# Kernel tuning notes

Hardware: AMD Instinct MI355X
Metric: run time of the kernel (lower is better)

The kernel has to match this reference:

```python
import jax, jax.numpy as jnp
import numpy as np

V, B, T, C, H, L = 32000, 4, 1024, 1024, 16, 8
HS = C // H  # head_size = 64


def _ln(x, g, b):
    m = x.mean(-1, keepdims=True)
    v = x.var(-1, keepdims=True)
    return (x - m) / jnp.sqrt(v + 1e-5) * g + b


def setup_inputs() -> dict:
    key = jax.random.key(0)
    ks = jax.random.split(key, 24)
    s = 0.02
    inp = {
        "idx": jax.random.randint(ks[0], (B, T), 0, V, dtype=jnp.int64),
        "tok_emb": jax.random.normal(ks[1], (V, C), jnp.float32) * s,
        "pos_emb": jax.random.normal(ks[2], (T, C), jnp.float32) * s,
        "Wq": jax.random.normal(ks[3], (L, H, C, HS), jnp.float32) * s,
        "Wk": jax.random.normal(ks[4], (L, H, C, HS), jnp.float32) * s,
        "Wv": jax.random.normal(ks[5], (L, H, C, HS), jnp.float32) * s,
        "Ph_w": jax.random.normal(ks[6], (L, H, HS, C), jnp.float32) * s,
        "Ph_b": jnp.zeros((L, H, C), jnp.float32),
        "Pm_w": jax.random.normal(ks[7], (L, C, C), jnp.float32) * s,
        "Pm_b": jnp.zeros((L, C), jnp.float32),
        "ln1_g": jnp.ones((L, C), jnp.float32),
        "ln1_b": jnp.zeros((L, C), jnp.float32),
        "ln2_g": jnp.ones((L, C), jnp.float32),
        "ln2_b": jnp.zeros((L, C), jnp.float32),
        "W1": jax.random.normal(ks[8], (L, C, 4 * C), jnp.float32) * s,
        "b1": jnp.zeros((L, 4 * C), jnp.float32),
        "W2": jax.random.normal(ks[9], (L, 4 * C, C), jnp.float32) * s,
        "b2": jnp.zeros((L, C), jnp.float32),
        "lnf_g": jnp.ones((C,), jnp.float32),
        "lnf_b": jnp.zeros((C,), jnp.float32),
        "head_w": jax.random.normal(ks[10], (C, V), jnp.float32) * s,
        "head_b": jnp.zeros((V,), jnp.float32),
    }
    return inp


def reference(idx, tok_emb, pos_emb, Wq, Wk, Wv, Ph_w, Ph_b, Pm_w, Pm_b,
              ln1_g, ln1_b, ln2_g, ln2_b, W1, b1, W2, b2, lnf_g, lnf_b,
              head_w, head_b):
    Bx, Tx = idx.shape
    x = tok_emb[idx] + pos_emb[:Tx]  # [B,T,C]
    mask = jnp.tril(jnp.ones((Tx, Tx), bool))
    scale = x.shape[-1] ** -0.5  # NOTE: original scales by n_embd**-0.5, not head_size
    n_layers = Wq.shape[0]
    for l in range(n_layers):
        xn = _ln(x, ln1_g[l], ln1_b[l])
        q = jnp.einsum('btc,hcs->bhts', xn, Wq[l])
        k = jnp.einsum('btc,hcs->bhts', xn, Wk[l])
        v = jnp.einsum('btc,hcs->bhts', xn, Wv[l])
        wei = jnp.einsum('bhts,bhus->bhtu', q, k) * scale
        wei = jnp.where(mask, wei, -jnp.inf)
        wei = jax.nn.softmax(wei, axis=-1)
        o = jnp.einsum('bhtu,bhus->bhts', wei, v)  # [B,H,T,HS]
        per = jnp.einsum('bhts,hsc->bhtc', o, Ph_w[l]) + Ph_b[l][None, :, None, :]
        sa = per.sum(axis=1) @ Pm_w[l] + Pm_b[l]  # combine heads, final proj
        x = x + sa
        xn2 = _ln(x, ln2_g[l], ln2_b[l])
        h = jax.nn.gelu(xn2 @ W1[l] + b1[l], approximate=False)
        x = x + h @ W2[l] + b2[l]
    x = _ln(x, lnf_g, lnf_b)
    return x @ head_w + head_b  # logits [B,T,V]
```

## Files before the change

kernel.cpp:

```cpp
#include <hip/hip_runtime.h>
#include <hip/hip_bf16.h>
#include <math.h>

static constexpr int V = 32000, B = 4, T = 1024, C = 1024, H = 16, NL = 8, HS = 64;
static constexpr int M = B * T;

typedef __bf16 bf16x8 __attribute__((ext_vector_type(8)));
typedef __bf16 bf16x4 __attribute__((ext_vector_type(4)));
typedef float f32x4 __attribute__((ext_vector_type(4)));

#define AS1 __attribute__((address_space(1)))
#define AS3 __attribute__((address_space(3)))

__global__ void k_embed(const int* __restrict__ idx, const float* __restrict__ tok,
                        const float* __restrict__ pos, float* __restrict__ x) {
  int g = blockIdx.x * blockDim.x + threadIdx.x;
  if (g >= M * C / 4) return;
  int c4 = g & 255;
  int bt = g >> 8;
  int t = bt & (T - 1);
  int row = idx[bt];
  float4 tv = *(const float4*)(tok + (size_t)row * C + c4 * 4);
  float4 pv = *(const float4*)(pos + (size_t)t * C + c4 * 4);
  float4 o;
  o.x = tv.x + pv.x; o.y = tv.y + pv.y; o.z = tv.z + pv.z; o.w = tv.w + pv.w;
  *(float4*)(x + (size_t)bt * C + c4 * 4) = o;
}

__global__ __launch_bounds__(256) void k_ln_bf(const float* __restrict__ x, const float* __restrict__ g,
                                               const float* __restrict__ b, __hip_bfloat16* __restrict__ y) {
  int row = blockIdx.x, tid = threadIdx.x;
  float4 v = ((const float4*)(x + (size_t)row * C))[tid];
  float s = v.x + v.y + v.z + v.w;
  float ss = v.x * v.x + v.y * v.y + v.z * v.z + v.w * v.w;
  for (int off = 32; off > 0; off >>= 1) {
    s += __shfl_down(s, off);
    ss += __shfl_down(ss, off);
  }
  __shared__ float sb[4], qb[4];
  int wid = tid >> 6;
  if ((tid & 63) == 0) { sb[wid] = s; qb[wid] = ss; }
  __syncthreads();
  float st = sb[0] + sb[1] + sb[2] + sb[3];
  float qt = qb[0] + qb[1] + qb[2] + qb[3];
  float mean = st * (1.0f / C);
  float var = qt * (1.0f / C) - mean * mean;
  float rstd = rsqrtf(var + 1e-5f);
  float4 gv = ((const float4*)g)[tid];
  float4 bv = ((const float4*)b)[tid];
  union { __hip_bfloat16 h[4]; ushort4 u; } pk;
  pk.h[0] = __float2bfloat16((v.x - mean) * rstd * gv.x + bv.x);
  pk.h[1] = __float2bfloat16((v.y - mean) * rstd * gv.y + bv.y);
  pk.h[2] = __float2bfloat16((v.z - mean) * rstd * gv.z + bv.z);
  pk.h[3] = __float2bfloat16((v.w - mean) * rstd * gv.w + bv.w);
  *(ushort4*)(y + (size_t)row * C + tid * 4) = pk.u;
}

__device__ __forceinline__ void transp_block(const float* __restrict__ in, __hip_bfloat16* __restrict__ out,
                                             int K, int N, int bx, int by, float (*t)[65]) {
  int n0 = bx * 64, k0 = by * 64;
  int tx = threadIdx.x & 15, ty = threadIdx.x >> 4;
#pragma unroll
  for (int i = 0; i < 64; i += 16) {
    float4 v = *(const float4*)(in + (size_t)(k0 + ty + i) * N + n0 + tx * 4);
    t[ty + i][tx * 4 + 0] = v.x;
    t[ty + i][tx * 4 + 1] = v.y;
    t[ty + i][tx * 4 + 2] = v.z;
    t[ty + i][tx * 4 + 3] = v.w;
  }
  __syncthreads();
#pragma unroll
  for (int i = 0; i < 64; i += 16) {
    int n = ty + i;
    union { __hip_bfloat16 h[4]; ushort4 u; } pk;
#pragma unroll
    for (int j = 0; j < 4; ++j) pk.h[j] = __float2bfloat16(t[tx * 4 + j][n]);
    *(ushort4*)(out + (size_t)(n0 + n) * K + k0 + tx * 4) = pk.u;
  }
}

__global__ __launch_bounds__(256) void k_transp(const float* __restrict__ in, __hip_bfloat16* __restrict__ out,
                                                int K, int N) {
  __shared__ float t[64][65];
  transp_block(in, out, K, N, blockIdx.x, blockIdx.y, t);
}

__global__ __launch_bounds__(256) void k_prep(const float* __restrict__ Wq, const float* __restrict__ Wk,
                                              const float* __restrict__ Wv, const float* __restrict__ Pm,
                                              const float* __restrict__ Ph, const float* __restrict__ W1,
                                              const float* __restrict__ W2,
                                              __hip_bfloat16* __restrict__ qkvw, __hip_bfloat16* __restrict__ pmT,
                                              __hip_bfloat16* __restrict__ phB, __hip_bfloat16* __restrict__ w1T,
                                              __hip_bfloat16* __restrict__ w2T) {
  __shared__ float tls[64][65];
  int bid = blockIdx.x;
  if (bid < 768) {
    int bx = bid & 15, z = bid >> 4;
    int sel = z >> 4, h = z & 15;
    const float* W = sel == 0 ? Wq : (sel == 1 ? Wk : Wv);
    const float* in = W + (size_t)h * C * HS;
    __hip_bfloat16* o = qkvw + ((size_t)sel * 1024 + h * 64) * C;
    int k0 = bx * 64;
    int tx = threadIdx.x & 15, ty = threadIdx.x >> 4;
#pragma unroll
    for (int i = 0; i < 64; i += 16) {
      float4 v = *(const float4*)(in + (size_t)(k0 + ty + i) * HS + tx * 4);
      tls[ty + i][tx * 4 + 0] = v.x;
      tls[ty + i][tx * 4 + 1] = v.y;
      tls[ty + i][tx * 4 + 2] = v.z;
      tls[ty + i][tx * 4 + 3] = v.w;
    }
    __syncthreads();
#pragma unroll
    for (int i = 0; i < 64; i += 16) {
      int n = ty + i;
      union { __hip_bfloat16 h4[4]; ushort4 u; } pk;
#pragma unroll
      for (int j = 0; j < 4; ++j) pk.h4[j] = __float2bfloat16(tls[tx * 4 + j][n]);
      *(ushort4*)(o + (size_t)n * C + k0 + tx * 4) = pk.u;
    }
  } else if (bid < 1024) {
    int r = bid - 768;
    transp_block(Pm, pmT, C, C, r & 15, r >> 4, tls);
  } else if (bid < 2048) {
    int g = (bid - 1024) * 256 + threadIdx.x;
    float4 v = ((const float4*)Ph)[g];
    union { __hip_bfloat16 h[4]; ushort4 u; } pk;
    pk.h[0] = __float2bfloat16(v.x);
    pk.h[1] = __float2bfloat16(v.y);
    pk.h[2] = __float2bfloat16(v.z);
    pk.h[3] = __float2bfloat16(v.w);
    ((ushort4*)phB)[g] = pk.u;
  } else if (bid < 3072) {
    int r = bid - 2048;
    transp_block(W1, w1T, C, 4 * C, r & 63, r >> 6, tls);
  } else {
    int r = bid - 3072;
    transp_block(W2, w2T, 4 * C, C, r & 15, r >> 4, tls);
  }
}

__global__ __launch_bounds__(256) void k_biasc(const float* __restrict__ phb, const float* __restrict__ Pm,
                                               const float* __restrict__ Pmb, float* __restrict__ bc) {
  __shared__ float bs[1024];
  __shared__ float red[4][64];
  int tid = threadIdx.x;
#pragma unroll
  for (int q = 0; q < 4; ++q) {
    int c = tid * 4 + q;
    float s = 0.0f;
    for (int h = 0; h < H; ++h) s += phb[(size_t)h * C + c];
    bs[c] = s;
  }
  __syncthreads();
  int c = blockIdx.x * 64 + (tid & 63);
  int part = tid >> 6;
  float s = 0.0f;
  for (int j = part * 256; j < part * 256 + 256; ++j) s += bs[j] * Pm[(size_t)j * C + c];
  red[part][tid & 63] = s;
  __syncthreads();
  if (tid < 64)
    bc[blockIdx.x * 64 + tid] = Pmb[blockIdx.x * 64 + tid] + red[0][tid] + red[1][tid] + red[2][tid] + red[3][tid];
}

template <int BIAS, int GELU, int RES, int OUTBF>
__global__ __launch_bounds__(256) void k_gemm_bf(const __hip_bfloat16* __restrict__ A,
                                                 const __hip_bfloat16* __restrict__ Bt,
                                                 void* Cout, const float* __restrict__ bias,
                                                 const float* res, int N, int K) {
  __shared__ __align__(16) __hip_bfloat16 As[128 * 32];
  __shared__ __align__(16) __hip_bfloat16 Bs[128 * 32];
  int bm = blockIdx.y * 128, bn = blockIdx.x * 128;
  int tid = threadIdx.x;
  int w = tid >> 6, l = tid & 63;
  int wr = (w >> 1) * 64, wc = (w & 1) * 64;
  int lr = l >> 2;
  int lk = (l & 3) * 8;
  int fr = l & 15;
  int fk = (l >> 4) * 8;
  const __hip_bfloat16* Ag = A + (size_t)bm * K;
  const __hip_bfloat16* Bg = Bt + (size_t)bn * K;
  f32x4 acc[4][4];
#pragma unroll
  for (int m = 0; m < 4; ++m)
#pragma unroll
    for (int n = 0; n < 4; ++n) acc[m][n] = (f32x4){0.f, 0.f, 0.f, 0.f};

  for (int k0 = 0; k0 < K; k0 += 32) {
    __syncthreads();
#pragma unroll
    for (int i = 0; i < 2; ++i) {
      int seg = w * 2 + i;
      int r = seg * 16 + lr;
      __builtin_amdgcn_global_load_lds((const AS1 void*)(Ag + (size_t)r * K + k0 + lk),
                                       (AS3 void*)(As + seg * 512), 16, 0, 0);
      __builtin_amdgcn_global_load_lds((const AS1 void*)(Bg + (size_t)r * K + k0 + lk),
                                       (AS3 void*)(Bs + seg * 512), 16, 0, 0);
    }
    __syncthreads();
    bf16x8 af[4], bfr[4];
#pragma unroll
    for (int m = 0; m < 4; ++m) af[m] = *(const bf16x8*)(As + ((size_t)(wr + m * 16 + fr)) * 32 + fk);
#pragma unroll
    for (int n = 0; n < 4; ++n) bfr[n] = *(const bf16x8*)(Bs + ((size_t)(wc + n * 16 + fr)) * 32 + fk);
#pragma unroll
    for (int m = 0; m < 4; ++m)
#pragma unroll
      for (int n = 0; n < 4; ++n)
        acc[m][n] = __builtin_amdgcn_mfma_f32_16x16x32_bf16(af[m], bfr[n], acc[m][n], 0, 0, 0);
  }
  int crow0 = (l >> 4) * 4;
  int ccol = l & 15;
#pragma unroll
  for (int m = 0; m < 4; ++m) {
    int row = bm + wr + m * 16 + crow0;
#pragma unroll
    for (int n = 0; n < 4; ++n) {
      int col = bn + wc + n * 16 + ccol;
      float bv = BIAS ? bias[col] : 0.0f;
#pragma unroll
      for (int r = 0; r < 4; ++r) {
        float v = acc[m][n][r] + bv;
        if (GELU) v = 0.5f * v * (1.0f + erff(v * 0.70710678118f));
        if (RES) v += res[(size_t)(row + r) * N + col];
        if (OUTBF)
          ((__hip_bfloat16*)Cout)[(size_t)(row + r) * N + col] = __float2bfloat16(v);
        else
          ((float*)Cout)[(size_t)(row + r) * N + col] = v;
      }
    }
  }
}

template <int BIAS, int GELU, int RES, int OUTBF>
__global__ __launch_bounds__(512, 2) void k_gemm256(const __hip_bfloat16* __restrict__ Ah,
                                                    const __hip_bfloat16* __restrict__ Bth,
                                                    void* Cout, const float* __restrict__ bias,
                                                    const float* res, int N, int K) {
  __shared__ __align__(16) __bf16 As[3][256 * 32];
  __shared__ __align__(16) __bf16 Bs[3][256 * 32];
  const __bf16* A = (const __bf16*)Ah;
  const __bf16* Bt = (const __bf16*)Bth;
  const int nx = N >> 8;
  const int bid = blockIdx.x;
  const int sw = ((bid & 7) * ((int)gridDim.x >> 3)) + (bid >> 3);
  const int bn = (sw % nx) << 8;
  const int bm = (sw / nx) << 8;
  const int tid = threadIdx.x, w = tid >> 6, l = tid & 63;
  const int wm = w >> 2, wn = w & 3;
  const int fr = l & 15, fg = l >> 4;
  const int srow = w * 32 + (l >> 2);
  const int scole = ((((l & 3) << 4) ^ ((l & 8) << 2) ^ (l & 16)) >> 1);
  const __bf16* Ag = A + (size_t)(bm + srow) * K + scole;
  const __bf16* Bg = Bt + (size_t)(bn + srow) * K + scole;
  const int arow = wm * 128 + fr;
  const int brow = wn * 64 + fr;
  const int koff = (((fg * 16) ^ (((fr & 2) << 4) | ((fr & 4) << 2))) >> 1);

  f32x4 acc[8][4];
#pragma unroll
  for (int m = 0; m < 8; ++m)
#pragma unroll
    for (int n = 0; n < 4; ++n) acc[m][n] = (f32x4){0.f, 0.f, 0.f, 0.f};

  auto stage = [&](int bufi, int tt) {
    size_t kb = (size_t)tt * 32;
#pragma unroll
    for (int jj = 0; jj < 2; ++jj) {
      __builtin_amdgcn_global_load_lds((const AS1 void*)(Ag + (size_t)jj * 16 * K + kb),
                                       (AS3 void*)(&As[bufi][(w * 32 + jj * 16) * 32]), 16, 0, 0);
      __builtin_amdgcn_global_load_lds((const AS1 void*)(Bg + (size_t)jj * 16 * K + kb),
                                       (AS3 void*)(&Bs[bufi][(w * 32 + jj * 16) * 32]), 16, 0, 0);
    }
  };

  const int NT = K >> 5;
  stage(0, 0);
  stage(1, 1);
  asm volatile("s_waitcnt vmcnt(4)" ::: "memory");
  __builtin_amdgcn_sched_barrier(0);
  __builtin_amdgcn_s_barrier();
  __builtin_amdgcn_sched_barrier(0);

  int cb = 0;
  for (int t = 0; t < NT; ++t) {
    int pb = cb + 2 >= 3 ? cb - 1 : cb + 2;
    if (t + 2 < NT) stage(pb, t + 2);
    bf16x8 fa[8], fb[4];
#pragma unroll
    for (int mg = 0; mg < 8; ++mg) fa[mg] = *(const bf16x8*)(&As[cb][(arow + mg * 16) * 32 + koff]);
#pragma unroll
    for (int ng = 0; ng < 4; ++ng) fb[ng] = *(const bf16x8*)(&Bs[cb][(brow + ng * 16) * 32 + koff]);
    __builtin_amdgcn_s_setprio(1);
#pragma unroll
    for (int mg = 0; mg < 8; ++mg)
#pragma unroll
      for (int ng = 0; ng < 4; ++ng)
        acc[mg][ng] = __builtin_amdgcn_mfma_f32_16x16x32_bf16(fa[mg], fb[ng], acc[mg][ng], 0, 0, 0);
    __builtin_amdgcn_s_setprio(0);
    if (t + 2 < NT)
      asm volatile("s_waitcnt vmcnt(4)" ::: "memory");
    else
      asm volatile("s_waitcnt vmcnt(0)" ::: "memory");
    __builtin_amdgcn_sched_barrier(0);
    __builtin_amdgcn_s_barrier();
    __builtin_amdgcn_sched_barrier(0);
    cb = cb + 1 >= 3 ? 0 : cb + 1;
  }

#pragma unroll
  for (int mg = 0; mg < 8; ++mg) {
    int row = bm + wm * 128 + mg * 16 + fg * 4;
#pragma unroll
    for (int n = 0; n < 4; ++n) {
      int col = bn + wn * 64 + n * 16 + fr;
      float bvx = BIAS ? bias[col] : 0.0f;
#pragma unroll
      for (int r = 0; r < 4; ++r) {
        float v = acc[mg][n][r] + bvx;
        if (GELU) v = 0.5f * v * (1.0f + erff(v * 0.70710678118f));
        if (RES) v += res[(size_t)(row + r) * N + col];
        if (OUTBF)
          ((__hip_bfloat16*)Cout)[(size_t)(row + r) * N + col] = __float2bfloat16(v);
        else
          ((float*)Cout)[(size_t)(row + r) * N + col] = v;
      }
    }
  }
}

__global__ __launch_bounds__(256) void k_attn(const __hip_bfloat16* __restrict__ qkvh,
                                              __hip_bfloat16* __restrict__ o) {
  const __bf16* qkv = (const __bf16*)qkvh;
  int qi = blockIdx.x;
  int bh = blockIdx.y;
  int b = bh >> 4, h = bh & 15;
  int tid = threadIdx.x;
  int w = tid >> 6, l = tid & 63;
  int fr = l & 15, fg = l >> 4;
  int qw = qi * 64 + w * 16;

  __shared__ __align__(16) __bf16 Ks[32][72];
  __shared__ __align__(16) __bf16 Vs[32][76];
  __shared__ __align__(16) __bf16 Ps[4][16][40];

  const size_t bT = (size_t)b * T;
  bf16x8 a_q[2];
  {
    const __bf16* qp = qkv + (bT + qw + fr) * 3072 + h * 64 + fg * 8;
    a_q[0] = *(const bf16x8*)qp;
    a_q[1] = *(const bf16x8*)(qp + 32);
  }
  f32x4 acc_o[4];
#pragma unroll
  for (int n = 0; n < 4; ++n) acc_o[n] = (f32x4){0.f, 0.f, 0.f, 0.f};
  float mrow[4] = {-1e30f, -1e30f, -1e30f, -1e30f};
  float lrow[4] = {0.f, 0.f, 0.f, 0.f};

  int sr = tid >> 3;
  int sc = (tid & 7) * 8;
  int ntile = (qi + 1) * 2;
  for (int t = 0; t < ntile; ++t) {
    int kv0 = t * 32;
    __syncthreads();
    {
      const __bf16* kp = qkv + (bT + kv0 + sr) * 3072 + 1024 + h * 64 + sc;
      bf16x8 k8 = *(const bf16x8*)kp;
      bf16x8 v8 = *(const bf16x8*)(kp + 1024);
      *(bf16x8*)&Ks[sr][sc] = k8;
      *(bf16x4*)&Vs[sr][sc] = __builtin_shufflevector(v8, v8, 0, 1, 2, 3);
      *(bf16x4*)&Vs[sr][sc + 4] = __builtin_shufflevector(v8, v8, 4, 5, 6, 7);
    }
    __syncthreads();
    if (kv0 > qw + 15) continue;

    f32x4 s0 = (f32x4){0.f, 0.f, 0.f, 0.f}, s1 = s0;
    s0 = __builtin_amdgcn_mfma_f32_16x16x32_bf16(a_q[0], *(const bf16x8*)&Ks[fr][fg * 8], s0, 0, 0, 0);
    s0 = __builtin_amdgcn_mfma_f32_16x16x32_bf16(a_q[1], *(const bf16x8*)&Ks[fr][32 + fg * 8], s0, 0, 0, 0);
    s1 = __builtin_amdgcn_mfma_f32_16x16x32_bf16(a_q[0], *(const bf16x8*)&Ks[16 + fr][fg * 8], s1, 0, 0, 0);
    s1 = __builtin_amdgcn_mfma_f32_16x16x32_bf16(a_q[1], *(const bf16x8*)&Ks[16 + fr][32 + fg * 8], s1, 0, 0, 0);

    int qrow = qw + fg * 4;
#pragma unroll
    for (int r = 0; r < 4; ++r) { s0[r] *= 0.03125f; s1[r] *= 0.03125f; }
    if (kv0 + 31 > qw) {
#pragma unroll
      for (int r = 0; r < 4; ++r) {
        if (kv0 + fr > qrow + r) s0[r] = -1e30f;
        if (kv0 + 16 + fr > qrow + r) s1[r] = -1e30f;
      }
    }
    float tm[4], psum[4], alpha[4];
#pragma unroll
    for (int r = 0; r < 4; ++r) tm[r] = fmaxf(s0[r], s1[r]);
#pragma unroll
    for (int off = 1; off < 16; off <<= 1)
#pragma unroll
      for (int r = 0; r < 4; ++r) tm[r] = fmaxf(tm[r], __shfl_xor(tm[r], off));
#pragma unroll
    for (int r = 0; r < 4; ++r) {
      float mnew = fmaxf(mrow[r], tm[r]);
      alpha[r] = __expf(mrow[r] - mnew);
      mrow[r] = mnew;
      float p0 = __expf(s0[r] - mnew);
      float p1 = __expf(s1[r] - mnew);
      s0[r] = p0; s1[r] = p1;
      psum[r] = p0 + p1;
    }
#pragma unroll
    for (int off = 1; off < 16; off <<= 1)
#pragma unroll
      for (int r = 0; r < 4; ++r) psum[r] += __shfl_xor(psum[r], off);
#pragma unroll
    for (int r = 0; r < 4; ++r) lrow[r] = lrow[r] * alpha[r] + psum[r];
#pragma unroll
    for (int n = 0; n < 4; ++n)
#pragma unroll
      for (int r = 0; r < 4; ++r) acc_o[n][r] *= alpha[r];

#pragma unroll
    for (int r = 0; r < 4; ++r) {
      Ps[w][fg * 4 + r][fr] = (__bf16)s0[r];
      Ps[w][fg * 4 + r][16 + fr] = (__bf16)s1[r];
    }
    bf16x8 a_p = *(const bf16x8*)&Ps[w][fr][fg * 8];
#pragma unroll
    for (int n = 0; n < 4; ++n) {
      bf16x8 bvv;
#pragma unroll
      for (int j = 0; j < 8; ++j) bvv[j] = Vs[fg * 8 + j][n * 16 + fr];
      acc_o[n] = __builtin_amdgcn_mfma_f32_16x16x32_bf16(a_p, bvv, acc_o[n], 0, 0, 0);
    }
  }
  float inv[4];
#pragma unroll
  for (int r = 0; r < 4; ++r) inv[r] = 1.0f / lrow[r];
  __bf16* ob = (__bf16*)o;
#pragma unroll
  for (int n = 0; n < 4; ++n)
#pragma unroll
    for (int r = 0; r < 4; ++r)
      ob[(bT + qw + fg * 4 + r) * 1024 + h * 64 + n * 16 + fr] = (__bf16)(acc_o[n][r] * inv[r]);
}

extern "C" void kernel_launch(void* const* d_in, const int* in_sizes, int n_in,
                              void* d_out, int out_size, void* d_ws, size_t ws_size,
                              hipStream_t stream) {
  const int* idx = (const int*)d_in[0];
  const float* tok = (const float*)d_in[1];
  const float* pos = (const float*)d_in[2];
  const float* Wq = (const float*)d_in[3];
  const float* Wk = (const float*)d_in[4];
  const float* Wv = (const float*)d_in[5];
  const float* Phw = (const float*)d_in[6];
  const float* Phb = (const float*)d_in[7];
  const float* Pmw = (const float*)d_in[8];
  const float* Pmb = (const float*)d_in[9];
  const float* ln1g = (const float*)d_in[10];
  const float* ln1b = (const float*)d_in[11];
  const float* ln2g = (const float*)d_in[12];
  const float* ln2b = (const float*)d_in[13];
  const float* W1 = (const float*)d_in[14];
  const float* b1 = (const float*)d_in[15];
  const float* W2 = (const float*)d_in[16];
  const float* b2 = (const float*)d_in[17];
  const float* lnfg = (const float*)d_in[18];
  const float* lnfb = (const float*)d_in[19];
  const float* headw = (const float*)d_in[20];
  const float* headb = (const float*)d_in[21];
  float* out = (float*)d_out;

  char* p = (char*)d_ws;
  float* x = (float*)p;                        p += (size_t)M * C * 4;
  float* bcv = (float*)p;                      p += 4096;
  char* layer_region = p;
  __hip_bfloat16* qkvb = (__hip_bfloat16*)p;   p += (size_t)M * 3072 * 2;
  __hip_bfloat16* ob = (__hip_bfloat16*)p;     p += (size_t)M * C * 2;
  __hip_bfloat16* hb = (__hip_bfloat16*)p;     p += (size_t)M * 4 * C * 2;
  __hip_bfloat16* xn = (__hip_bfloat16*)p;     p += (size_t)M * C * 2;
  __hip_bfloat16* qkvw = (__hip_bfloat16*)p;   p += (size_t)3 * C * C * 2;
  __hip_bfloat16* pmT = (__hip_bfloat16*)p;    p += (size_t)C * C * 2;
  __hip_bfloat16* phB = (__hip_bfloat16*)p;    p += (size_t)C * C * 2;
  __hip_bfloat16* wcombT = (__hip_bfloat16*)p; p += (size_t)C * C * 2;
  __hip_bfloat16* w1T = (__hip_bfloat16*)p;    p += (size_t)4 * C * C * 2;
  __hip_bfloat16* w2T = (__hip_bfloat16*)p;    p += (size_t)4 * C * C * 2;
  __hip_bfloat16* wt_head = (__hip_bfloat16*)layer_region;

  k_embed<<<(M * C / 4 + 255) / 256, 256, 0, stream>>>(idx, tok, pos, x);

  for (int l = 0; l < NL; ++l) {
    k_ln_bf<<<M, 256, 0, stream>>>(x, ln1g + (size_t)l * C, ln1b + (size_t)l * C, xn);
    k_prep<<<4096, 256, 0, stream>>>(Wq + (size_t)l * H * C * HS, Wk + (size_t)l * H * C * HS,
                                     Wv + (size_t)l * H * C * HS, Pmw + (size_t)l * C * C,
                                     Phw + (size_t)l * H * HS * C, W1 + (size_t)l * C * 4 * C,
                                     W2 + (size_t)l * 4 * C * C, qkvw, pmT, phB, w1T, w2T);
    k_gemm256<0, 0, 0, 1><<<(3072 / 256) * (M / 256), 512, 0, stream>>>(xn, qkvw, qkvb, nullptr, nullptr, 3072, C);
    k_attn<<<dim3(T / 64, B * H), 256, 0, stream>>>(qkvb, ob);
    k_biasc<<<16, 256, 0, stream>>>(Phb + (size_t)l * H * C, Pmw + (size_t)l * C * C, Pmb + (size_t)l * C, bcv);
    k_gemm_bf<0, 0, 0, 1><<<dim3(C / 128, C / 128), 256, 0, stream>>>(pmT, phB, wcombT, nullptr, nullptr, C, C);
    k_gemm_bf<1, 0, 1, 0><<<dim3(C / 128, M / 128), 256, 0, stream>>>(ob, wcombT, x, bcv, x, C, C);
    k_ln_bf<<<M, 256, 0, stream>>>(x, ln2g + (size_t)l * C, ln2b + (size_t)l * C, xn);
    k_gemm256<1, 1, 0, 1><<<(4 * C / 256) * (M / 256), 512, 0, stream>>>(xn, w1T, hb, b1 + (size_t)l * 4 * C, nullptr, 4 * C, C);
    k_gemm_bf<1, 0, 1, 0><<<dim3(C / 128, M / 128), 256, 0, stream>>>(hb, w2T, x, b2 + (size_t)l * C, x, C, 4 * C);
  }

  k_ln_bf<<<M, 256, 0, stream>>>(x, lnfg, lnfb, xn);
  k_transp<<<dim3(500, 16), 256, 0, stream>>>(headw, wt_head, C, V);
  k_gemm256<1, 0, 0, 0><<<(V / 256) * (M / 256), 512, 0, stream>>>(xn, wt_head, out, headb, nullptr, V, C);
}
```

Baseline: 3.837 ms.

## Deepen GEMM LDS pipeline to four stages with register double-buffered fragments

Grows the 256x256 GEMM shared-memory ring from three to four buffers and prefetches three K-tiles ahead instead of two. LDS fragment reads for the next tile are issued into a second register set before the MFMAs on the current set, so LDS reads overlap matrix math. The cost is more shared memory, which with two blocks per CU at launch bounds (512,2) may limit occupancy, plus higher register pressure from the doubled fragment arrays. The unrolled loop steps by two tiles and assumes an even K-tile count.

```diff
diff --git a/kernel.cpp b/kernel.cpp
--- a/kernel.cpp
+++ b/kernel.cpp
@@ -237,8 +237,8 @@
                                                     const __hip_bfloat16* __restrict__ Bth,
                                                     void* Cout, const float* __restrict__ bias,
                                                     const float* res, int N, int K) {
-  __shared__ __align__(16) __bf16 As[3][256 * 32];
-  __shared__ __align__(16) __bf16 Bs[3][256 * 32];
+  __shared__ __align__(16) __bf16 As[4][256 * 32];
+  __shared__ __align__(16) __bf16 Bs[4][256 * 32];
   const __bf16* A = (const __bf16*)Ah;
   const __bf16* Bt = (const __bf16*)Bth;
   const int nx = N >> 8;
@@ -274,39 +274,58 @@
     }
   };
 
+  bf16x8 fa[2][8], fb[2][4];
+
+#define READF(SET, BI)                                                              \
+  {                                                                                 \
+    const int bi_ = (BI);                                                           \
+    _Pragma("unroll") for (int mg = 0; mg < 8; ++mg)                                \
+        fa[SET][mg] = *(const bf16x8*)(&As[bi_][(arow + mg * 16) * 32 + koff]);     \
+    _Pragma("unroll") for (int ng = 0; ng < 4; ++ng)                                \
+        fb[SET][ng] = *(const bf16x8*)(&Bs[bi_][(brow + ng * 16) * 32 + koff]);     \
+  }
+
+#define MFMAS(SET)                                                                  \
+  _Pragma("unroll") for (int mg = 0; mg < 8; ++mg)                                  \
+      _Pragma("unroll") for (int ng = 0; ng < 4; ++ng)                              \
+          acc[mg][ng] =                                                             \
+              __builtin_amdgcn_mfma_f32_16x16x32_bf16(fa[SET][mg], fb[SET][ng], acc[mg][ng], 0, 0, 0);
+
+#define GITER(T, CUR, NXT)                                                          \
+  {                                                                                 \
+    const int t_ = (T);                                                             \
+    asm volatile("s_waitcnt lgkmcnt(0)" ::: "memory");                              \
+    if (t_ + 2 < NT)                                                                \
+      asm volatile("s_waitcnt vmcnt(4)" ::: "memory");                              \
+    else                                                                            \
+      asm volatile("s_waitcnt vmcnt(0)" ::: "memory");                              \
+    __builtin_amdgcn_sched_barrier(0);                                              \
+    __builtin_amdgcn_s_barrier();                                                   \
+    __builtin_amdgcn_sched_barrier(0);                                              \
+    if (t_ + 1 < NT) READF(NXT, (t_ + 1) & 3);                                      \
+    if (t_ + 3 < NT) stage((t_ + 3) & 3, t_ + 3);                                   \
+    __builtin_amdgcn_s_setprio(1);                                                  \
+    MFMAS(CUR);                                                                     \
+    __builtin_amdgcn_s_setprio(0);                                                  \
+  }
+
   const int NT = K >> 5;
   stage(0, 0);
   stage(1, 1);
-  asm volatile("s_waitcnt vmcnt(4)" ::: "memory");
+  stage(2, 2);
+  asm volatile("s_waitcnt vmcnt(8)" ::: "memory");
   __builtin_amdgcn_sched_barrier(0);
   __builtin_amdgcn_s_barrier();
   __builtin_amdgcn_sched_barrier(0);
-
-  int cb = 0;
-  for (int t = 0; t < NT; ++t) {
-    int pb = cb + 2 >= 3 ? cb - 1 : cb + 2;
-    if (t + 2 < NT) stage(pb, t + 2);
-    bf16x8 fa[8], fb[4];
-#pragma unroll
-    for (int mg = 0; mg < 8; ++mg) fa[mg] = *(const bf16x8*)(&As[cb][(arow + mg * 16) * 32 + koff]);
-#pragma unroll
-    for (int ng = 0; ng < 4; ++ng) fb[ng] = *(const bf16x8*)(&Bs[cb][(brow + ng * 16) * 32 + koff]);
-    __builtin_amdgcn_s_setprio(1);
-#pragma unroll
-    for (int mg = 0; mg < 8; ++mg)
-#pragma unroll
-      for (int ng = 0; ng < 4; ++ng)
-        acc[mg][ng] = __builtin_amdgcn_mfma_f32_16x16x32_bf16(fa[mg], fb[ng], acc[mg][ng], 0, 0, 0);
-    __builtin_amdgcn_s_setprio(0);
-    if (t + 2 < NT)
-      asm volatile("s_waitcnt vmcnt(4)" ::: "memory");
-    else
-      asm volatile("s_waitcnt vmcnt(0)" ::: "memory");
-    __builtin_amdgcn_sched_barrier(0);
-    __builtin_amdgcn_s_barrier();
-    __builtin_amdgcn_sched_barrier(0);
-    cb = cb + 1 >= 3 ? 0 : cb + 1;
-  }
+  READF(0, 0);
+
+  for (int t = 0; t < NT; t += 2) {
+    GITER(t, 0, 1);
+    GITER(t + 1, 1, 0);
+  }
+#undef READF
+#undef MFMAS
+#undef GITER
 
 #pragma unroll
   for (int mg = 0; mg < 8; ++mg) {
```

Result: faster. 3.596 ms (-6.3%).
